# Kernel optimization log

Measured on AMD Instinct MI355X. Metric: run time of the kernel, lower is better.

## Reference

```python
import jax, jax.numpy as jnp
import numpy as np

CAPACITY_FACTOR = 1.0
MIN_CAPACITY = 4


def setup_inputs() -> dict:
    key = jax.random.key(0)
    ks = jax.random.split(key, 4)
    B, S, D, E, F = 4, 2048, 1024, 16, 4096
    hidden_states = jax.random.normal(ks[0], (B, S, D), dtype=jnp.float32)
    wg = jax.random.normal(ks[1], (D, E), dtype=jnp.float32) * 0.02
    w1 = jax.random.normal(ks[2], (E, D, F), dtype=jnp.float32) * (1.0 / np.sqrt(D))
    b1 = jnp.zeros((E, F), dtype=jnp.float32)
    w2 = jax.random.normal(ks[3], (E, F, D), dtype=jnp.float32) * (1.0 / np.sqrt(F))
    b2 = jnp.zeros((E, D), dtype=jnp.float32)
    return {"hidden_states": hidden_states, "wg": wg, "w1": w1, "b1": b1, "w2": w2, "b2": b2}


def reference(hidden_states, wg, w1, b1, w2, b2):
    B, S, D = hidden_states.shape
    x = hidden_states.reshape(-1, D)                      # [T, D] tokens
    T = x.shape[0]
    E = wg.shape[1]
    capacity = max(int(np.ceil(T / E * CAPACITY_FACTOR)), MIN_CAPACITY)  # static

    # ---- TopKGate (k=1, no noise, no RTS) ----
    logits = x @ wg                                       # [T, E]
    gates = jax.nn.softmax(logits, axis=-1)
    idx1 = jnp.argmax(gates, axis=1)                      # [T]
    mask1 = jax.nn.one_hot(idx1, E, dtype=gates.dtype)    # [T, E]
    exp_counts = jnp.sum(mask1, axis=0).astype(jnp.int32) # per-expert token counts

    # load-balancing aux loss
    me = jnp.mean(gates, axis=0)
    ce = jnp.mean(mask1, axis=0)
    l_aux = jnp.sum(me * ce) * E

    # slot assignment within each expert, drop overflow tokens
    locations1 = jnp.cumsum(mask1, axis=0) - 1.0          # [T, E]
    mask1 = mask1 * (locations1 < capacity).astype(gates.dtype)
    locations1_s = jnp.sum(locations1 * mask1, axis=1).astype(jnp.int32)  # [T]
    gates1 = gates * mask1                                # [T, E] gate prob of kept assignment

    loc_oh = jax.nn.one_hot(locations1_s, capacity, dtype=gates.dtype)    # [T, C]
    combine = jnp.einsum('te,tc->tec', gates1, loc_oh)    # [T, E, C]
    dispatch = (combine > 0).astype(x.dtype)              # [T, E, C]

    # ---- dispatch -> grouped expert FFN -> combine ----
    disp = jnp.einsum('tec,td->ecd', dispatch, x)         # [E, C, D]
    h = jax.nn.gelu(jnp.einsum('ecd,edf->ecf', disp, w1) + b1[:, None, :])
    eo = jnp.einsum('ecf,efd->ecd', h, w2) + b2[:, None, :]  # [E, C, D]
    out = jnp.einsum('tec,ecd->td', combine, eo).reshape(B, S, D)
    return out, l_aux, exp_counts
```

## Files before the change

kernel.cpp:

```cpp
#include <hip/hip_runtime.h>

typedef unsigned short u16;
typedef unsigned int   u32;
typedef unsigned long long u64;
typedef __attribute__((ext_vector_type(8))) __bf16 bf16x8;
typedef __attribute__((ext_vector_type(4))) float  f32x4;

#define TOK 8192
#define DIM 1024
#define NE  16
#define NF  4096
#define CAP 512

__device__ __forceinline__ u16 f2bf(float f) {
    u32 u = __float_as_uint(f);
    u32 r = (u + 0x7FFFu + ((u >> 16) & 1u)) >> 16;
    return (u16)r;
}

__device__ __forceinline__ float gelu_tanh(float x) {
    float u = 0.7978845608028654f * (x + 0.044715f * x * x * x);
    float t = __expf(-2.f * fabsf(u));
    float th = (1.f - t) / (1.f + t);
    th = (u < 0.f) ? -th : th;
    return 0.5f * x * (1.f + th);
}

__device__ __forceinline__ void gld16(const void* g, void* l) {
    __builtin_amdgcn_global_load_lds(
        (const __attribute__((address_space(1))) void*)g,
        (__attribute__((address_space(3))) void*)l, 16, 0, 0);
}

__global__ void moe_wgT(const float* __restrict__ wg, float* __restrict__ wgT,
                        float* __restrict__ me_sums) {
    int i = blockIdx.x * 256 + threadIdx.x;
    if (i < NE) me_sums[i] = 0.f;
    int d = i >> 4, e = i & 15;
    wgT[(size_t)e * DIM + d] = wg[i];
}

__global__ void moe_gate(const float* __restrict__ x, const float* __restrict__ wgT,
                         int* __restrict__ eidx, float* __restrict__ gp,
                         float* __restrict__ me_sums) {
    __shared__ float lme[NE];
    const int tid = threadIdx.x;
    if (tid < NE) lme[tid] = 0.f;
    __syncthreads();
    const int tok = blockIdx.x * 16 + (tid >> 4);
    const int e   = tid & 15;
    const float4* xp = (const float4*)(x + (size_t)tok * DIM);
    const float4* wp = (const float4*)(wgT + (size_t)e * DIM);
    float acc = 0.f;
#pragma unroll 4
    for (int i = 0; i < DIM / 4; ++i) {
        float4 a = xp[i], b = wp[i];
        acc = fmaf(a.x, b.x, acc); acc = fmaf(a.y, b.y, acc);
        acc = fmaf(a.z, b.z, acc); acc = fmaf(a.w, b.w, acc);
    }
    float mx = acc;
    for (int off = 8; off; off >>= 1) mx = fmaxf(mx, __shfl_xor(mx, off, 16));
    float ex = __expf(acc - mx);
    float sum = ex;
    for (int off = 8; off; off >>= 1) sum += __shfl_xor(sum, off, 16);
    float p = ex / sum;
    atomicAdd(&lme[e], p);
    float bv = acc; int bi = e;
    for (int off = 8; off; off >>= 1) {
        float ov = __shfl_xor(bv, off, 16);
        int   oi = __shfl_xor(bi, off, 16);
        if (ov > bv || (ov == bv && oi < bi)) { bv = ov; bi = oi; }
    }
    float pw = __shfl(p, bi, 16);
    if (e == 0) { eidx[tok] = bi; gp[tok] = pw; }
    __syncthreads();
    if (tid < 16) atomicAdd(&me_sums[tid], lme[tid]);
}

__global__ void moe_scan(const int* __restrict__ eidx, const float* __restrict__ me_sums,
                         int* __restrict__ slot, int* __restrict__ tos,
                         float* __restrict__ tail ) {
    __shared__ int wcnt[16][16];
    __shared__ int base[16];
    const int tid = threadIdx.x, wid = tid >> 6, lane = tid & 63;
    if (tid < 16) base[tid] = 0;
    for (int i = tid; i < NE * CAP; i += 1024) tos[i] = -1;
    __syncthreads();
    const u64 below = ((u64)1 << lane) - 1;
    for (int chunk = 0; chunk < TOK / 1024; ++chunk) {
        int t = chunk * 1024 + tid;
        int e = eidx[t];
        int rank = 0;
#pragma unroll
        for (int ex = 0; ex < 16; ++ex) {
            u64 m = __ballot(e == ex);
            if (e == ex)    rank = __popcll(m & below);
            if (lane == ex) wcnt[wid][ex] = __popcll(m);
        }
        __syncthreads();
        int pre = base[e];
        for (int w = 0; w < wid; ++w) pre += wcnt[w][e];
        int s = pre + rank;
        slot[t] = s;
        if (s < CAP) tos[e * CAP + s] = t;
        __syncthreads();
        if (tid < 16) {
            int tot = 0;
            for (int w = 0; w < 16; ++w) tot += wcnt[w][tid];
            base[tid] += tot;
        }
        __syncthreads();
    }
    if (tid == 0) {
        float laux = 0.f;
        for (int e2 = 0; e2 < 16; ++e2) {
            float me = me_sums[e2] / (float)TOK;
            float ce = (float)base[e2] / (float)TOK;
            laux += me * ce;
        }
        tail[0] = laux * (float)NE;
    }
    if (tid < 16) tail[1 + tid] = (float)base[tid];
}

__global__ void moe_gather_zero(const float* __restrict__ x, const int* __restrict__ tos,
                                const int* __restrict__ slot, u16* __restrict__ Xg,
                                float* __restrict__ out) {
    const int b = blockIdx.x, tid = threadIdx.x;
    const int t = tos[b];
    float4 v = make_float4(0.f, 0.f, 0.f, 0.f);
    if (t >= 0) v = *(const float4*)(x + (size_t)t * DIM + tid * 4);
    u32 lo = (u32)f2bf(v.x) | ((u32)f2bf(v.y) << 16);
    u32 hi = (u32)f2bf(v.z) | ((u32)f2bf(v.w) << 16);
    *(uint2*)(Xg + (size_t)b * DIM + tid * 4) = make_uint2(lo, hi);
    if (slot[b] >= CAP)
        *(float4*)(out + (size_t)b * DIM + tid * 4) = make_float4(0.f, 0.f, 0.f, 0.f);
}

__global__ void moe_convT(const float* __restrict__ src, u16* __restrict__ dst,
                          int R, int C) {
    __shared__ float tile[64][65];
    int b = blockIdx.x;
    const int tilesC = C >> 6, tilesR = R >> 6;
    int tc = b % tilesC; b /= tilesC;
    int tr = b % tilesR; int e = b / tilesR;
    const float* S = src + ((size_t)e * R + tr * 64) * C + tc * 64;
    const int tid = threadIdx.x;
    const int rr = tid >> 4, cc = (tid & 15) * 4;
#pragma unroll
    for (int i = 0; i < 4; ++i) {
        float4 v = *(const float4*)(S + (size_t)(rr + i * 16) * C + cc);
        tile[rr + i * 16][cc + 0] = v.x; tile[rr + i * 16][cc + 1] = v.y;
        tile[rr + i * 16][cc + 2] = v.z; tile[rr + i * 16][cc + 3] = v.w;
    }
    __syncthreads();
    const int c = tid >> 2, r0 = (tid & 3) * 16;
    u16 tmp[16];
#pragma unroll
    for (int k = 0; k < 16; ++k) tmp[k] = f2bf(tile[r0 + k][c]);
    u16* D = dst + ((size_t)e * C + tc * 64 + c) * R + tr * 64 + r0;
    uint4 w0 = make_uint4((u32)tmp[0] | ((u32)tmp[1] << 16), (u32)tmp[2] | ((u32)tmp[3] << 16),
                          (u32)tmp[4] | ((u32)tmp[5] << 16), (u32)tmp[6] | ((u32)tmp[7] << 16));
    uint4 w1 = make_uint4((u32)tmp[8] | ((u32)tmp[9] << 16), (u32)tmp[10] | ((u32)tmp[11] << 16),
                          (u32)tmp[12] | ((u32)tmp[13] << 16), (u32)tmp[14] | ((u32)tmp[15] << 16));
    *(uint4*)(D) = w0;
    *(uint4*)(D + 8) = w1;
}

__global__ __launch_bounds__(512, 4) void moe_gemm1cv(const u16* __restrict__ Xg,
                                                      const u16* __restrict__ W1t,
                                                      const float* __restrict__ b1,
                                                      u16* __restrict__ H,
                                                      const float* __restrict__ w2,
                                                      u16* __restrict__ W2t) {
    __shared__ alignas(16) char smem[49152];
    const int bid = blockIdx.x;
    const int tid = threadIdx.x;
    if (bid % 5 == 0) {
        u16* Als = (u16*)smem;
        u16* Bls = (u16*)(smem + 32768);
        const int g    = bid / 5;
        const int wave = tid >> 6, lane = tid & 63;
        const int xcd  = bid & 7;
        const int h    = g >> 3;
        const int e    = xcd * 2 + (h >> 6);
        const int tl   = h & 63;
        const int bm   = tl & 1;
        const int bn   = tl >> 1;
        const int r4   = lane >> 2;
        const int gch  = (lane & 3) ^ ((lane >> 3) & 3);
        const u16* aSrc = Xg + (size_t)(e * 512 + bm * 256 + wave * 16 + r4) * DIM + gch * 8;
        const u16* bSrc = W1t + (size_t)e * NF * DIM
                        + (size_t)(bn * 128 + wave * 16 + r4) * DIM + gch * 8;
        const int wm = wave & 1, wn = wave >> 1;
        const int fr = lane & 15, fq = lane >> 4;
        const int rdoff = fr * 32 + (fq ^ ((fr >> 1) & 3)) * 8;
        f32x4 acc[2][4][2] = {};

#define STG1(P, T) do { const int ko = (T) * 32; \
        u16* ad = Als + (P) * 8192 + wave * 512; \
        u16* bd = Bls + (P) * 4096 + wave * 512; \
        gld16(aSrc + ko, ad); gld16(aSrc + 128 * DIM + ko, ad + 4096); \
        gld16(bSrc + ko, bd); } while (0)

        const int NT = DIM / 32;
        STG1(0, 0);
        asm volatile("s_waitcnt vmcnt(0)" ::: "memory");
        __builtin_amdgcn_s_barrier();
        int cur = 0;
        for (int t = 0; t < NT; ++t) {
            if (t + 1 < NT) STG1(cur ^ 1, t + 1);
            const u16* Ab = Als + cur * 8192;
            const u16* Bb = Bls + cur * 4096;
            bf16x8 aF[4], bF[2];
#pragma unroll
            for (int j = 0; j < 2; ++j)
                bF[j] = *(const bf16x8*)(const void*)(Bb + (wn * 32 + j * 16) * 32 + rdoff);
#pragma unroll
            for (int i = 0; i < 4; ++i)
                aF[i] = *(const bf16x8*)(const void*)(Ab + (wm * 128 + i * 16) * 32 + rdoff);
            __builtin_amdgcn_s_setprio(1);
#pragma unroll
            for (int i = 0; i < 4; ++i)
#pragma unroll
                for (int j = 0; j < 2; ++j)
                    acc[0][i][j] = __builtin_amdgcn_mfma_f32_16x16x32_bf16(aF[i], bF[j], acc[0][i][j], 0, 0, 0);
            __builtin_amdgcn_s_setprio(0);
#pragma unroll
            for (int i = 0; i < 4; ++i)
                aF[i] = *(const bf16x8*)(const void*)(Ab + (wm * 128 + 64 + i * 16) * 32 + rdoff);
            __builtin_amdgcn_s_setprio(1);
#pragma unroll
            for (int i = 0; i < 4; ++i)
#pragma unroll
                for (int j = 0; j < 2; ++j)
                    acc[1][i][j] = __builtin_amdgcn_mfma_f32_16x16x32_bf16(aF[i], bF[j], acc[1][i][j], 0, 0, 0);
            __builtin_amdgcn_s_setprio(0);
            asm volatile("s_waitcnt vmcnt(0)" ::: "memory");
            __builtin_amdgcn_s_barrier();
            cur ^= 1;
        }
#undef STG1
        const int mBase = e * 512 + bm * 256 + wm * 128;
        const int nBase = bn * 128 + wn * 32;
#pragma unroll
        for (int j = 0; j < 2; ++j) {
            const int f = nBase + j * 16 + fr;
            const float bias = b1[e * NF + f];
#pragma unroll
            for (int q = 0; q < 2; ++q)
#pragma unroll
                for (int i = 0; i < 4; ++i) {
                    const int m0 = mBase + q * 64 + i * 16 + fq * 4;
#pragma unroll
                    for (int r = 0; r < 4; ++r) {
                        float v = acc[q][i][j][r] + bias;
                        H[(size_t)(m0 + r) * NF + f] = f2bf(gelu_tanh(v));
                    }
                }
        }
    } else {
        float (*tA)[65] = (float(*)[65])smem;
        float (*tB)[65] = (float(*)[65])(smem + 16640);
        const int cid  = bid - bid / 5 - 1;
        const int sub  = tid >> 8, stid = tid & 255;
        float (*tl)[65] = sub ? tB : tA;
        const int R = NF, C = DIM, tilesC = C >> 6, tilesR = R >> 6;
#pragma unroll
        for (int kk = 0; kk < 2; ++kk) {
            int ob = cid * 4 + sub * 2 + kk;
            int tc = ob % tilesC; int bb = ob / tilesC;
            int tr = bb % tilesR; int e = bb / tilesR;
            const float* S = w2 + ((size_t)e * R + tr * 64) * C + tc * 64;
            const int rr = stid >> 4, cc = (stid & 15) * 4;
#pragma unroll
            for (int i = 0; i < 4; ++i) {
                float4 v = *(const float4*)(S + (size_t)(rr + i * 16) * C + cc);
                tl[rr + i * 16][cc + 0] = v.x; tl[rr + i * 16][cc + 1] = v.y;
                tl[rr + i * 16][cc + 2] = v.z; tl[rr + i * 16][cc + 3] = v.w;
            }
            __syncthreads();
            const int c = stid >> 2, r0 = (stid & 3) * 16;
            u16 tmp[16];
#pragma unroll
            for (int k2 = 0; k2 < 16; ++k2) tmp[k2] = f2bf(tl[r0 + k2][c]);
            u16* D = W2t + ((size_t)e * C + tc * 64 + c) * R + tr * 64 + r0;
            uint4 w0 = make_uint4((u32)tmp[0] | ((u32)tmp[1] << 16), (u32)tmp[2] | ((u32)tmp[3] << 16),
                                  (u32)tmp[4] | ((u32)tmp[5] << 16), (u32)tmp[6] | ((u32)tmp[7] << 16));
            uint4 w1 = make_uint4((u32)tmp[8] | ((u32)tmp[9] << 16), (u32)tmp[10] | ((u32)tmp[11] << 16),
                                  (u32)tmp[12] | ((u32)tmp[13] << 16), (u32)tmp[14] | ((u32)tmp[15] << 16));
            *(uint4*)(D) = w0;
            *(uint4*)(D + 8) = w1;
            __syncthreads();
        }
    }
}

__global__ __launch_bounds__(512, 2) void moe_gemm2(const u16* __restrict__ H,
                                                    const u16* __restrict__ W2t,
                                                    const float* __restrict__ b2,
                                                    const int* __restrict__ tos,
                                                    const float* __restrict__ gp,
                                                    float* __restrict__ out) {
    __shared__ alignas(16) u16 Als[4][8192];
    __shared__ alignas(16) u16 Bls[4][4096];
    const int tid = threadIdx.x, wave = tid >> 6, lane = tid & 63;
    const int flat = blockIdx.x;
    const int xcd  = flat & 7;
    const int slot = flat >> 3;
    const int e    = xcd * 2 + (slot >> 4);
    const int tile = slot & 15;
    const int bm   = tile & 1;
    const int bn   = tile >> 1;
    const int r4   = lane >> 2;
    const int gch  = (lane & 3) ^ ((lane >> 3) & 3);
    const u16* aSrc = H + (size_t)(e * 512 + bm * 256 + wave * 16 + r4) * NF + gch * 8;
    const u16* bSrc = W2t + (size_t)e * DIM * NF
                    + (size_t)(bn * 128 + wave * 16 + r4) * NF + gch * 8;
    const int wm = wave & 1, wn = wave >> 1;
    const int fr = lane & 15, fq = lane >> 4;
    const int rdoff = fr * 32 + (fq ^ ((fr >> 1) & 3)) * 8;

    f32x4 acc[2][4][2] = {};

#define STG2A(P, T) do { const int ko = (T) * 32; u16* ad = &Als[P][wave * 512]; \
        gld16(aSrc + ko, ad); gld16(aSrc + (size_t)128 * NF + ko, ad + 4096); } while (0)
#define STG2B(P, T) do { const int ko = (T) * 32; u16* bd = &Bls[P][wave * 512]; \
        gld16(bSrc + ko, bd); } while (0)

    const int NT = NF / 32;
    STG2A(0, 0); STG2B(0, 0);
    STG2A(1, 1); STG2B(1, 1);
    STG2A(2, 2); STG2B(2, 2);
    for (int t = 0; t < NT; ++t) {
        const int c = t & 3;
        const int rem = NT - 1 - t;
        if (rem >= 2)      asm volatile("s_waitcnt vmcnt(6)" ::: "memory");
        else if (rem == 1) asm volatile("s_waitcnt vmcnt(3)" ::: "memory");
        else               asm volatile("s_waitcnt vmcnt(0)" ::: "memory");
        __builtin_amdgcn_sched_barrier(0);
        __builtin_amdgcn_s_barrier();
        __builtin_amdgcn_sched_barrier(0);
        const u16* Ab = &Als[c][0];
        const u16* Bb = &Bls[c][0];
        bf16x8 bF[2], aF[4];
#pragma unroll
        for (int j = 0; j < 2; ++j)
            bF[j] = *(const bf16x8*)(const void*)(Bb + (wn * 32 + j * 16) * 32 + rdoff);
#pragma unroll
        for (int i = 0; i < 4; ++i)
            aF[i] = *(const bf16x8*)(const void*)(Ab + (wm * 128 + i * 16) * 32 + rdoff);
        if (t + 3 < NT) STG2A((c + 3) & 3, t + 3);
        __builtin_amdgcn_sched_barrier(0);
        asm volatile("s_waitcnt lgkmcnt(0)" ::: "memory");
        __builtin_amdgcn_sched_barrier(0);
        __builtin_amdgcn_s_setprio(1);
#pragma unroll
        for (int i = 0; i < 4; ++i)
#pragma unroll
            for (int j = 0; j < 2; ++j)
                acc[0][i][j] = __builtin_amdgcn_mfma_f32_16x16x32_bf16(aF[i], bF[j], acc[0][i][j], 0, 0, 0);
        __builtin_amdgcn_s_setprio(0);
        __builtin_amdgcn_sched_barrier(0);
        __builtin_amdgcn_s_barrier();
        __builtin_amdgcn_sched_barrier(0);
#pragma unroll
        for (int i = 0; i < 4; ++i)
            aF[i] = *(const bf16x8*)(const void*)(Ab + (wm * 128 + 64 + i * 16) * 32 + rdoff);
        if (t + 3 < NT) STG2B((c + 3) & 3, t + 3);
        __builtin_amdgcn_sched_barrier(0);
        asm volatile("s_waitcnt lgkmcnt(0)" ::: "memory");
        __builtin_amdgcn_sched_barrier(0);
        __builtin_amdgcn_s_setprio(1);
#pragma unroll
        for (int i = 0; i < 4; ++i)
#pragma unroll
            for (int j = 0; j < 2; ++j)
                acc[1][i][j] = __builtin_amdgcn_mfma_f32_16x16x32_bf16(aF[i], bF[j], acc[1][i][j], 0, 0, 0);
        __builtin_amdgcn_s_setprio(0);
    }
#undef STG2A
#undef STG2B

    const int mBase = e * 512 + bm * 256 + wm * 128;
    const int nBase = bn * 128 + wn * 32;
#pragma unroll
    for (int q = 0; q < 2; ++q)
#pragma unroll
        for (int i = 0; i < 4; ++i) {
#pragma unroll
            for (int r = 0; r < 4; ++r) {
                const int m = mBase + q * 64 + i * 16 + fq * 4 + r;
                const int t = tos[m];
                if (t < 0) continue;
                const float g = gp[t];
#pragma unroll
                for (int j = 0; j < 2; ++j) {
                    const int d = nBase + j * 16 + fr;
                    out[(size_t)t * DIM + d] = g * (acc[q][i][j][r] + b2[e * DIM + d]);
                }
            }
        }
}

extern "C" void kernel_launch(void* const* d_in, const int* in_sizes, int n_in,
                              void* d_out, int out_size, void* d_ws, size_t ws_size,
                              hipStream_t stream) {
    const float* x  = (const float*)d_in[0];
    const float* wg = (const float*)d_in[1];
    const float* w1 = (const float*)d_in[2];
    const float* b1 = (const float*)d_in[3];
    const float* w2 = (const float*)d_in[4];
    const float* b2 = (const float*)d_in[5];
    float* out = (float*)d_out;

    char* ws = (char*)d_ws;
    const size_t W1_OFF  = 0;
    const size_t W2_OFF  = W1_OFF + (size_t)NE * NF * DIM * 2;
    const size_t XG_OFF  = W2_OFF + (size_t)NE * NF * DIM * 2;
    const size_t H_OFF   = XG_OFF + (size_t)TOK * DIM * 2;
    const size_t SM_OFF  = H_OFF + (size_t)TOK * NF * 2;
    u16* W1bf = (u16*)(ws + W1_OFF);
    u16* W2bf = (u16*)(ws + W2_OFF);
    u16* Xg   = (u16*)(ws + XG_OFF);
    u16* H    = (u16*)(ws + H_OFF);
    int*   eidx = (int*)(ws + SM_OFF);
    float* gp   = (float*)(ws + SM_OFF + 32768);
    int*   slot = (int*)(ws + SM_OFF + 65536);
    int*   tos  = (int*)(ws + SM_OFF + 98304);
    float* me   = (float*)(ws + SM_OFF + 131072);
    float* wgT  = (float*)(ws + SM_OFF + 131072 + 128);

    float* tail = out + (size_t)TOK * DIM;

    moe_wgT<<<64, 256, 0, stream>>>(wg, wgT, me);
    moe_gate<<<TOK / 16, 256, 0, stream>>>(x, wgT, eidx, gp, me);
    moe_scan<<<1, 1024, 0, stream>>>(eidx, me, slot, tos, tail);
    moe_gather_zero<<<NE * CAP, 256, 0, stream>>>(x, tos, slot, Xg, out);
    moe_convT<<<NE * (DIM / 64) * (NF / 64), 256, 0, stream>>>(w1, W1bf, DIM, NF);
    moe_gemm1cv<<<5120, 512, 0, stream>>>(Xg, W1bf, b1, H, w2, W2bf);
    moe_gemm2<<<256, 512, 0, stream>>>(H, W2bf, b2, tos, gp, out);
}
```

Before: 889.7 us.

## Fuse fp32 weight conversion into GEMM loads using LDS transpose reads

Drops the separate weight transpose/convert passes (moe_convT and the w2 conversion blocks folded into gemm1). Both GEMMs now read fp32 weights directly, convert them to bf16 in registers, and store them to a padded LDS layout. B fragments are then read with ds_read_b64_tr_b16 transpose loads. This removes the write and re-read of about 256 MB of bf16 weight copies. The cost is doubled fp32 weight read bytes inside the GEMMs and register-staged loads. gemm2 also goes from a 4-stage async pipeline to a 2-stage synchronous one, which may expose more latency.

```diff
diff --git a/kernel.cpp b/kernel.cpp
--- a/kernel.cpp
+++ b/kernel.cpp
@@ -5,12 +5,17 @@
 typedef unsigned long long u64;
 typedef __attribute__((ext_vector_type(8))) __bf16 bf16x8;
 typedef __attribute__((ext_vector_type(4))) float  f32x4;
+typedef __attribute__((ext_vector_type(2))) u32    u32x2;
 
 #define TOK 8192
 #define DIM 1024
 #define NE  16
 #define NF  4096
 #define CAP 512
+
+#define BQ  288
+#define BG  1184
+#define BLSZ 9472
 
 __device__ __forceinline__ u16 f2bf(float f) {
     u32 u = __float_as_uint(f);
@@ -31,6 +36,24 @@
         (const __attribute__((address_space(1))) void*)g,
         (__attribute__((address_space(3))) void*)l, 16, 0, 0);
 }
+
+__device__ __forceinline__ u32 lds_addr(const void* p) {
+    return (u32)(uintptr_t)(const __attribute__((address_space(3))) void*)p;
+}
+
+#define BFRAG2(BF0, BF1, A0, A1) do { \
+    u32x2 l0_, h0_, l1_, h1_; \
+    asm volatile("ds_read_b64_tr_b16 %0, %4\n\t" \
+                 "ds_read_b64_tr_b16 %1, %4 offset:128\n\t" \
+                 "ds_read_b64_tr_b16 %2, %5\n\t" \
+                 "ds_read_b64_tr_b16 %3, %5 offset:128\n\t" \
+                 "s_waitcnt lgkmcnt(0)" \
+                 : "=&v"(l0_), "=&v"(h0_), "=&v"(l1_), "=&v"(h1_) \
+                 : "v"(A0), "v"(A1) : "memory"); \
+    union { u32 u[4]; bf16x8 v; } c0_, c1_; \
+    c0_.u[0] = l0_[0]; c0_.u[1] = l0_[1]; c0_.u[2] = h0_[0]; c0_.u[3] = h0_[1]; \
+    c1_.u[0] = l1_[0]; c1_.u[1] = l1_[1]; c1_.u[2] = h1_[0]; c1_.u[3] = h1_[1]; \
+    (BF0) = c0_.v; (BF1) = c1_.v; } while (0)
 
 __global__ void moe_wgT(const float* __restrict__ wg, float* __restrict__ wgT,
                         float* __restrict__ me_sums) {
@@ -137,173 +160,123 @@
         *(float4*)(out + (size_t)b * DIM + tid * 4) = make_float4(0.f, 0.f, 0.f, 0.f);
 }
 
-__global__ void moe_convT(const float* __restrict__ src, u16* __restrict__ dst,
-                          int R, int C) {
-    __shared__ float tile[64][65];
-    int b = blockIdx.x;
-    const int tilesC = C >> 6, tilesR = R >> 6;
-    int tc = b % tilesC; b /= tilesC;
-    int tr = b % tilesR; int e = b / tilesR;
-    const float* S = src + ((size_t)e * R + tr * 64) * C + tc * 64;
-    const int tid = threadIdx.x;
-    const int rr = tid >> 4, cc = (tid & 15) * 4;
-#pragma unroll
-    for (int i = 0; i < 4; ++i) {
-        float4 v = *(const float4*)(S + (size_t)(rr + i * 16) * C + cc);
-        tile[rr + i * 16][cc + 0] = v.x; tile[rr + i * 16][cc + 1] = v.y;
-        tile[rr + i * 16][cc + 2] = v.z; tile[rr + i * 16][cc + 3] = v.w;
-    }
-    __syncthreads();
-    const int c = tid >> 2, r0 = (tid & 3) * 16;
-    u16 tmp[16];
-#pragma unroll
-    for (int k = 0; k < 16; ++k) tmp[k] = f2bf(tile[r0 + k][c]);
-    u16* D = dst + ((size_t)e * C + tc * 64 + c) * R + tr * 64 + r0;
-    uint4 w0 = make_uint4((u32)tmp[0] | ((u32)tmp[1] << 16), (u32)tmp[2] | ((u32)tmp[3] << 16),
-                          (u32)tmp[4] | ((u32)tmp[5] << 16), (u32)tmp[6] | ((u32)tmp[7] << 16));
-    uint4 w1 = make_uint4((u32)tmp[8] | ((u32)tmp[9] << 16), (u32)tmp[10] | ((u32)tmp[11] << 16),
-                          (u32)tmp[12] | ((u32)tmp[13] << 16), (u32)tmp[14] | ((u32)tmp[15] << 16));
-    *(uint4*)(D) = w0;
-    *(uint4*)(D + 8) = w1;
-}
-
-__global__ __launch_bounds__(512, 4) void moe_gemm1cv(const u16* __restrict__ Xg,
-                                                      const u16* __restrict__ W1t,
-                                                      const float* __restrict__ b1,
-                                                      u16* __restrict__ H,
-                                                      const float* __restrict__ w2,
-                                                      u16* __restrict__ W2t) {
-    __shared__ alignas(16) char smem[49152];
-    const int bid = blockIdx.x;
-    const int tid = threadIdx.x;
-    if (bid % 5 == 0) {
-        u16* Als = (u16*)smem;
-        u16* Bls = (u16*)(smem + 32768);
-        const int g    = bid / 5;
-        const int wave = tid >> 6, lane = tid & 63;
-        const int xcd  = bid & 7;
-        const int h    = g >> 3;
-        const int e    = xcd * 2 + (h >> 6);
-        const int tl   = h & 63;
-        const int bm   = tl & 1;
-        const int bn   = tl >> 1;
-        const int r4   = lane >> 2;
-        const int gch  = (lane & 3) ^ ((lane >> 3) & 3);
-        const u16* aSrc = Xg + (size_t)(e * 512 + bm * 256 + wave * 16 + r4) * DIM + gch * 8;
-        const u16* bSrc = W1t + (size_t)e * NF * DIM
-                        + (size_t)(bn * 128 + wave * 16 + r4) * DIM + gch * 8;
-        const int wm = wave & 1, wn = wave >> 1;
-        const int fr = lane & 15, fq = lane >> 4;
-        const int rdoff = fr * 32 + (fq ^ ((fr >> 1) & 3)) * 8;
-        f32x4 acc[2][4][2] = {};
-
-#define STG1(P, T) do { const int ko = (T) * 32; \
-        u16* ad = Als + (P) * 8192 + wave * 512; \
-        u16* bd = Bls + (P) * 4096 + wave * 512; \
-        gld16(aSrc + ko, ad); gld16(aSrc + 128 * DIM + ko, ad + 4096); \
-        gld16(bSrc + ko, bd); } while (0)
-
-        const int NT = DIM / 32;
-        STG1(0, 0);
-        asm volatile("s_waitcnt vmcnt(0)" ::: "memory");
+__global__ __launch_bounds__(512, 4) void moe_gemm1(const u16* __restrict__ Xg,
+                                                    const float* __restrict__ w1,
+                                                    const float* __restrict__ b1,
+                                                    u16* __restrict__ H) {
+    __shared__ alignas(16) u16 Als[2][8192];
+    __shared__ alignas(16) u16 Bls[2][BLSZ / 2];
+    const int tid = threadIdx.x, wave = tid >> 6, lane = tid & 63;
+    const int flat = blockIdx.x;
+    const int xcd  = flat & 7;
+    const int slot = flat >> 3;
+    const int e    = xcd * 2 + (slot >> 6);
+    const int tile = slot & 63;
+    const int bm   = tile & 1;
+    const int bn   = tile >> 1;
+    const int r4   = lane >> 2;
+    const int gch  = (lane & 3) ^ ((lane >> 3) & 3);
+    const u16* aSrc = Xg + (size_t)(e * 512 + bm * 256 + wave * 16 + r4) * DIM + gch * 8;
+    const int bk = tid >> 4, bn8 = tid & 15;
+    const float* bSrc = w1 + ((size_t)e * DIM + bk) * NF + bn * 128 + bn8 * 8;
+    const int bwoff = (bn8 >> 1) * BG + (bk >> 3) * BQ + (bk & 7) * 32 + (bn8 & 1) * 16;
+    const int wm = wave & 1, wn = wave >> 1;
+    const int fr = lane & 15, fq = lane >> 4;
+    const int rdoff = fr * 32 + (fq ^ ((fr >> 1) & 3)) * 8;
+    const u32 ldsB = lds_addr(&Bls[0][0]);
+    const int btr0 = (wn * 2 + 0) * BG + fq * BQ + fr * 2;
+    const int btr1 = (wn * 2 + 1) * BG + fq * BQ + fr * 2;
+
+    f32x4 acc[2][4][2] = {};
+    float4 q0, q1;
+
+#define STGA1(P, T) do { const int ko = (T) * 32; \
+        u16* ad = &Als[P][wave * 512]; \
+        gld16(aSrc + ko, ad); gld16(aSrc + 128 * DIM + ko, ad + 4096); } while (0)
+#define BWR1(P) do { \
+        u32 p0 = (u32)f2bf(q0.x) | ((u32)f2bf(q0.y) << 16); \
+        u32 p1 = (u32)f2bf(q0.z) | ((u32)f2bf(q0.w) << 16); \
+        u32 p2 = (u32)f2bf(q1.x) | ((u32)f2bf(q1.y) << 16); \
+        u32 p3 = (u32)f2bf(q1.z) | ((u32)f2bf(q1.w) << 16); \
+        *(uint4*)((char*)&Bls[0][0] + (P) * BLSZ + bwoff) = make_uint4(p0, p1, p2, p3); } while (0)
+
+    const int NT = DIM / 32;
+    STGA1(0, 0);
+    q0 = *(const float4*)(bSrc); q1 = *(const float4*)(bSrc + 4);
+    asm volatile("s_waitcnt vmcnt(0)" ::: "memory");
+    BWR1(0);
+    asm volatile("s_waitcnt lgkmcnt(0)" ::: "memory");
+    __builtin_amdgcn_s_barrier();
+    for (int t = 0; t < NT; ++t) {
+        const int buf = t & 1;
+        if (t + 1 < NT) {
+            STGA1(buf ^ 1, t + 1);
+            const float* s = bSrc + (size_t)(t + 1) * (32 * NF);
+            q0 = *(const float4*)(s); q1 = *(const float4*)(s + 4);
+        }
+        bf16x8 aF[4], bF[2];
+        const u32 bb = ldsB + buf * BLSZ;
+        BFRAG2(bF[0], bF[1], bb + btr0, bb + btr1);
+        const u16* Ab = &Als[buf][0];
+#pragma unroll
+        for (int i = 0; i < 4; ++i)
+            aF[i] = *(const bf16x8*)(const void*)(Ab + (wm * 128 + i * 16) * 32 + rdoff);
+        __builtin_amdgcn_sched_barrier(0);
+        __builtin_amdgcn_s_setprio(1);
+#pragma unroll
+        for (int i = 0; i < 4; ++i)
+#pragma unroll
+            for (int j = 0; j < 2; ++j)
+                acc[0][i][j] = __builtin_amdgcn_mfma_f32_16x16x32_bf16(aF[i], bF[j], acc[0][i][j], 0, 0, 0);
+        __builtin_amdgcn_s_setprio(0);
+#pragma unroll
+        for (int i = 0; i < 4; ++i)
+            aF[i] = *(const bf16x8*)(const void*)(Ab + (wm * 128 + 64 + i * 16) * 32 + rdoff);
+        __builtin_amdgcn_s_setprio(1);
+#pragma unroll
+        for (int i = 0; i < 4; ++i)
+#pragma unroll
+            for (int j = 0; j < 2; ++j)
+                acc[1][i][j] = __builtin_amdgcn_mfma_f32_16x16x32_bf16(aF[i], bF[j], acc[1][i][j], 0, 0, 0);
+        __builtin_amdgcn_s_setprio(0);
+        if (t + 1 < NT) {
+            asm volatile("s_waitcnt vmcnt(0)" ::: "memory");
+            BWR1(buf ^ 1);
+        }
+        asm volatile("s_waitcnt lgkmcnt(0)" ::: "memory");
         __builtin_amdgcn_s_barrier();
-        int cur = 0;
-        for (int t = 0; t < NT; ++t) {
-            if (t + 1 < NT) STG1(cur ^ 1, t + 1);
-            const u16* Ab = Als + cur * 8192;
-            const u16* Bb = Bls + cur * 4096;
-            bf16x8 aF[4], bF[2];
-#pragma unroll
-            for (int j = 0; j < 2; ++j)
-                bF[j] = *(const bf16x8*)(const void*)(Bb + (wn * 32 + j * 16) * 32 + rdoff);
-#pragma unroll
-            for (int i = 0; i < 4; ++i)
-                aF[i] = *(const bf16x8*)(const void*)(Ab + (wm * 128 + i * 16) * 32 + rdoff);
-            __builtin_amdgcn_s_setprio(1);
-#pragma unroll
-            for (int i = 0; i < 4; ++i)
-#pragma unroll
-                for (int j = 0; j < 2; ++j)
-                    acc[0][i][j] = __builtin_amdgcn_mfma_f32_16x16x32_bf16(aF[i], bF[j], acc[0][i][j], 0, 0, 0);
-            __builtin_amdgcn_s_setprio(0);
-#pragma unroll
-            for (int i = 0; i < 4; ++i)
-                aF[i] = *(const bf16x8*)(const void*)(Ab + (wm * 128 + 64 + i * 16) * 32 + rdoff);
-            __builtin_amdgcn_s_setprio(1);
-#pragma unroll
-            for (int i = 0; i < 4; ++i)
-#pragma unroll
-                for (int j = 0; j < 2; ++j)
-                    acc[1][i][j] = __builtin_amdgcn_mfma_f32_16x16x32_bf16(aF[i], bF[j], acc[1][i][j], 0, 0, 0);
-            __builtin_amdgcn_s_setprio(0);
-            asm volatile("s_waitcnt vmcnt(0)" ::: "memory");
-            __builtin_amdgcn_s_barrier();
-            cur ^= 1;
-        }
-#undef STG1
-        const int mBase = e * 512 + bm * 256 + wm * 128;
-        const int nBase = bn * 128 + wn * 32;
-#pragma unroll
-        for (int j = 0; j < 2; ++j) {
-            const int f = nBase + j * 16 + fr;
-            const float bias = b1[e * NF + f];
-#pragma unroll
-            for (int q = 0; q < 2; ++q)
-#pragma unroll
-                for (int i = 0; i < 4; ++i) {
-                    const int m0 = mBase + q * 64 + i * 16 + fq * 4;
-#pragma unroll
-                    for (int r = 0; r < 4; ++r) {
-                        float v = acc[q][i][j][r] + bias;
-                        H[(size_t)(m0 + r) * NF + f] = f2bf(gelu_tanh(v));
-                    }
+    }
+#undef STGA1
+#undef BWR1
+
+    const int mBase = e * 512 + bm * 256 + wm * 128;
+    const int nBase = bn * 128 + wn * 32;
+#pragma unroll
+    for (int j = 0; j < 2; ++j) {
+        const int f = nBase + j * 16 + fr;
+        const float bias = b1[e * NF + f];
+#pragma unroll
+        for (int q = 0; q < 2; ++q)
+#pragma unroll
+            for (int i = 0; i < 4; ++i) {
+                const int m0 = mBase + q * 64 + i * 16 + fq * 4;
+#pragma unroll
+                for (int r = 0; r < 4; ++r) {
+                    float v = acc[q][i][j][r] + bias;
+                    H[(size_t)(m0 + r) * NF + f] = f2bf(gelu_tanh(v));
                 }
-        }
-    } else {
-        float (*tA)[65] = (float(*)[65])smem;
-        float (*tB)[65] = (float(*)[65])(smem + 16640);
-        const int cid  = bid - bid / 5 - 1;
-        const int sub  = tid >> 8, stid = tid & 255;
-        float (*tl)[65] = sub ? tB : tA;
-        const int R = NF, C = DIM, tilesC = C >> 6, tilesR = R >> 6;
-#pragma unroll
-        for (int kk = 0; kk < 2; ++kk) {
-            int ob = cid * 4 + sub * 2 + kk;
-            int tc = ob % tilesC; int bb = ob / tilesC;
-            int tr = bb % tilesR; int e = bb / tilesR;
-            const float* S = w2 + ((size_t)e * R + tr * 64) * C + tc * 64;
-            const int rr = stid >> 4, cc = (stid & 15) * 4;
-#pragma unroll
-            for (int i = 0; i < 4; ++i) {
-                float4 v = *(const float4*)(S + (size_t)(rr + i * 16) * C + cc);
-                tl[rr + i * 16][cc + 0] = v.x; tl[rr + i * 16][cc + 1] = v.y;
-                tl[rr + i * 16][cc + 2] = v.z; tl[rr + i * 16][cc + 3] = v.w;
             }
-            __syncthreads();
-            const int c = stid >> 2, r0 = (stid & 3) * 16;
-            u16 tmp[16];
-#pragma unroll
-            for (int k2 = 0; k2 < 16; ++k2) tmp[k2] = f2bf(tl[r0 + k2][c]);
-            u16* D = W2t + ((size_t)e * C + tc * 64 + c) * R + tr * 64 + r0;
-            uint4 w0 = make_uint4((u32)tmp[0] | ((u32)tmp[1] << 16), (u32)tmp[2] | ((u32)tmp[3] << 16),
-                                  (u32)tmp[4] | ((u32)tmp[5] << 16), (u32)tmp[6] | ((u32)tmp[7] << 16));
-            uint4 w1 = make_uint4((u32)tmp[8] | ((u32)tmp[9] << 16), (u32)tmp[10] | ((u32)tmp[11] << 16),
-                                  (u32)tmp[12] | ((u32)tmp[13] << 16), (u32)tmp[14] | ((u32)tmp[15] << 16));
-            *(uint4*)(D) = w0;
-            *(uint4*)(D + 8) = w1;
-            __syncthreads();
-        }
-    }
-}
-
-__global__ __launch_bounds__(512, 2) void moe_gemm2(const u16* __restrict__ H,
-                                                    const u16* __restrict__ W2t,
+    }
+}
+
+__global__ __launch_bounds__(512, 4) void moe_gemm2(const u16* __restrict__ H,
+                                                    const float* __restrict__ w2,
                                                     const float* __restrict__ b2,
                                                     const int* __restrict__ tos,
                                                     const float* __restrict__ gp,
                                                     float* __restrict__ out) {
-    __shared__ alignas(16) u16 Als[4][8192];
-    __shared__ alignas(16) u16 Bls[4][4096];
+    __shared__ alignas(16) u16 Als[2][8192];
+    __shared__ alignas(16) u16 Bls[2][BLSZ / 2];
     const int tid = threadIdx.x, wave = tid >> 6, lane = tid & 63;
     const int flat = blockIdx.x;
     const int xcd  = flat & 7;
@@ -315,44 +288,50 @@
     const int r4   = lane >> 2;
     const int gch  = (lane & 3) ^ ((lane >> 3) & 3);
     const u16* aSrc = H + (size_t)(e * 512 + bm * 256 + wave * 16 + r4) * NF + gch * 8;
-    const u16* bSrc = W2t + (size_t)e * DIM * NF
-                    + (size_t)(bn * 128 + wave * 16 + r4) * NF + gch * 8;
+    const int bk = tid >> 4, bn8 = tid & 15;
+    const float* bSrc = w2 + ((size_t)e * NF + bk) * DIM + bn * 128 + bn8 * 8;
+    const int bwoff = (bn8 >> 1) * BG + (bk >> 3) * BQ + (bk & 7) * 32 + (bn8 & 1) * 16;
     const int wm = wave & 1, wn = wave >> 1;
     const int fr = lane & 15, fq = lane >> 4;
     const int rdoff = fr * 32 + (fq ^ ((fr >> 1) & 3)) * 8;
+    const u32 ldsB = lds_addr(&Bls[0][0]);
+    const int btr0 = (wn * 2 + 0) * BG + fq * BQ + fr * 2;
+    const int btr1 = (wn * 2 + 1) * BG + fq * BQ + fr * 2;
 
     f32x4 acc[2][4][2] = {};
-
-#define STG2A(P, T) do { const int ko = (T) * 32; u16* ad = &Als[P][wave * 512]; \
+    float4 q0, q1;
+
+#define STGA2(P, T) do { const int ko = (T) * 32; \
+        u16* ad = &Als[P][wave * 512]; \
         gld16(aSrc + ko, ad); gld16(aSrc + (size_t)128 * NF + ko, ad + 4096); } while (0)
-#define STG2B(P, T) do { const int ko = (T) * 32; u16* bd = &Bls[P][wave * 512]; \
-        gld16(bSrc + ko, bd); } while (0)
+#define BWR2(P) do { \
+        u32 p0 = (u32)f2bf(q0.x) | ((u32)f2bf(q0.y) << 16); \
+        u32 p1 = (u32)f2bf(q0.z) | ((u32)f2bf(q0.w) << 16); \
+        u32 p2 = (u32)f2bf(q1.x) | ((u32)f2bf(q1.y) << 16); \
+        u32 p3 = (u32)f2bf(q1.z) | ((u32)f2bf(q1.w) << 16); \
+        *(uint4*)((char*)&Bls[0][0] + (P) * BLSZ + bwoff) = make_uint4(p0, p1, p2, p3); } while (0)
 
     const int NT = NF / 32;
-    STG2A(0, 0); STG2B(0, 0);
-    STG2A(1, 1); STG2B(1, 1);
-    STG2A(2, 2); STG2B(2, 2);
+    STGA2(0, 0);
+    q0 = *(const float4*)(bSrc); q1 = *(const float4*)(bSrc + 4);
+    asm volatile("s_waitcnt vmcnt(0)" ::: "memory");
+    BWR2(0);
+    asm volatile("s_waitcnt lgkmcnt(0)" ::: "memory");
+    __builtin_amdgcn_s_barrier();
     for (int t = 0; t < NT; ++t) {
-        const int c = t & 3;
-        const int rem = NT - 1 - t;
-        if (rem >= 2)      asm volatile("s_waitcnt vmcnt(6)" ::: "memory");
-        else if (rem == 1) asm volatile("s_waitcnt vmcnt(3)" ::: "memory");
-        else               asm volatile("s_waitcnt vmcnt(0)" ::: "memory");
-        __builtin_amdgcn_sched_barrier(0);
-        __builtin_amdgcn_s_barrier();
-        __builtin_amdgcn_sched_barrier(0);
-        const u16* Ab = &Als[c][0];
-        const u16* Bb = &Bls[c][0];
-        bf16x8 bF[2], aF[4];
-#pragma unroll
-        for (int j = 0; j < 2; ++j)
-            bF[j] = *(const bf16x8*)(const void*)(Bb + (wn * 32 + j * 16) * 32 + rdoff);
+        const int buf = t & 1;
+        if (t + 1 < NT) {
+            STGA2(buf ^ 1, t + 1);
+            const float* s = bSrc + (size_t)(t + 1) * (32 * DIM);
+            q0 = *(const float4*)(s); q1 = *(const float4*)(s + 4);
+        }
+        bf16x8 aF[4], bF[2];
+        const u32 bb = ldsB + buf * BLSZ;
+        BFRAG2(bF[0], bF[1], bb + btr0, bb + btr1);
+        const u16* Ab = &Als[buf][0];
 #pragma unroll
         for (int i = 0; i < 4; ++i)
             aF[i] = *(const bf16x8*)(const void*)(Ab + (wm * 128 + i * 16) * 32 + rdoff);
-        if (t + 3 < NT) STG2A((c + 3) & 3, t + 3);
-        __builtin_amdgcn_sched_barrier(0);
-        asm volatile("s_waitcnt lgkmcnt(0)" ::: "memory");
         __builtin_amdgcn_sched_barrier(0);
         __builtin_amdgcn_s_setprio(1);
 #pragma unroll
@@ -361,16 +340,9 @@
             for (int j = 0; j < 2; ++j)
                 acc[0][i][j] = __builtin_amdgcn_mfma_f32_16x16x32_bf16(aF[i], bF[j], acc[0][i][j], 0, 0, 0);
         __builtin_amdgcn_s_setprio(0);
-        __builtin_amdgcn_sched_barrier(0);
-        __builtin_amdgcn_s_barrier();
-        __builtin_amdgcn_sched_barrier(0);
 #pragma unroll
         for (int i = 0; i < 4; ++i)
             aF[i] = *(const bf16x8*)(const void*)(Ab + (wm * 128 + 64 + i * 16) * 32 + rdoff);
-        if (t + 3 < NT) STG2B((c + 3) & 3, t + 3);
-        __builtin_amdgcn_sched_barrier(0);
-        asm volatile("s_waitcnt lgkmcnt(0)" ::: "memory");
-        __builtin_amdgcn_sched_barrier(0);
         __builtin_amdgcn_s_setprio(1);
 #pragma unroll
         for (int i = 0; i < 4; ++i)
@@ -378,9 +350,15 @@
             for (int j = 0; j < 2; ++j)
                 acc[1][i][j] = __builtin_amdgcn_mfma_f32_16x16x32_bf16(aF[i], bF[j], acc[1][i][j], 0, 0, 0);
         __builtin_amdgcn_s_setprio(0);
-    }
-#undef STG2A
-#undef STG2B
+        if (t + 1 < NT) {
+            asm volatile("s_waitcnt vmcnt(0)" ::: "memory");
+            BWR2(buf ^ 1);
+        }
+        asm volatile("s_waitcnt lgkmcnt(0)" ::: "memory");
+        __builtin_amdgcn_s_barrier();
+    }
+#undef STGA2
+#undef BWR2
 
     const int mBase = e * 512 + bm * 256 + wm * 128;
     const int nBase = bn * 128 + wn * 32;
@@ -415,15 +393,11 @@
     float* out = (float*)d_out;
 
     char* ws = (char*)d_ws;
-    const size_t W1_OFF  = 0;
-    const size_t W2_OFF  = W1_OFF + (size_t)NE * NF * DIM * 2;
-    const size_t XG_OFF  = W2_OFF + (size_t)NE * NF * DIM * 2;
-    const size_t H_OFF   = XG_OFF + (size_t)TOK * DIM * 2;
-    const size_t SM_OFF  = H_OFF + (size_t)TOK * NF * 2;
-    u16* W1bf = (u16*)(ws + W1_OFF);
-    u16* W2bf = (u16*)(ws + W2_OFF);
-    u16* Xg   = (u16*)(ws + XG_OFF);
-    u16* H    = (u16*)(ws + H_OFF);
+    const size_t XG_OFF = 0;
+    const size_t H_OFF  = XG_OFF + (size_t)TOK * DIM * 2;
+    const size_t SM_OFF = H_OFF + (size_t)TOK * NF * 2;
+    u16* Xg = (u16*)(ws + XG_OFF);
+    u16* H  = (u16*)(ws + H_OFF);
     int*   eidx = (int*)(ws + SM_OFF);
     float* gp   = (float*)(ws + SM_OFF + 32768);
     int*   slot = (int*)(ws + SM_OFF + 65536);
@@ -437,7 +411,6 @@
     moe_gate<<<TOK / 16, 256, 0, stream>>>(x, wgT, eidx, gp, me);
     moe_scan<<<1, 1024, 0, stream>>>(eidx, me, slot, tos, tail);
     moe_gather_zero<<<NE * CAP, 256, 0, stream>>>(x, tos, slot, Xg, out);
-    moe_convT<<<NE * (DIM / 64) * (NF / 64), 256, 0, stream>>>(w1, W1bf, DIM, NF);
-    moe_gemm1cv<<<5120, 512, 0, stream>>>(Xg, W1bf, b1, H, w2, W2bf);
-    moe_gemm2<<<256, 512, 0, stream>>>(H, W2bf, b2, tos, gp, out);
-}
+    moe_gemm1<<<1024, 512, 0, stream>>>(Xg, w1, b1, H);
+    moe_gemm2<<<256, 512, 0, stream>>>(H, w2, b2, tos, gp, out);
+}
```

Result: faster. 808.5 us (-9.1%).
